# Optimization experiments

Measured on AMD Instinct MI355X. Metric: run time of the kernel, lower is better.

The kernel has to match this reference:

```python
import jax, jax.numpy as jnp
import numpy as np

N = 250_000          # total nodes
D = 256              # emb_size
B = 8_192            # number of graphs in batch


def setup_inputs() -> dict:
    key = jax.random.key(0)
    k1, k2, k3 = jax.random.split(key, 3)
    node_rep = jax.random.normal(k1, (N, D), dtype=jnp.float32)
    batch = jnp.sort(jax.random.randint(k2, (N,), 0, B, dtype=jnp.int32))
    # labels in [-1, 4); -1 marks 'condition' (reactant-context) nodes
    primary_label = jax.random.randint(k3, (N,), 0, 5, dtype=jnp.int32) - 1
    return {"node_rep": node_rep, "batch": batch,
            "primary_label": primary_label, "num_graphs": B}


def reference(node_rep, batch, primary_label, num_graphs):
    n = node_rep.shape[0]
    mask = primary_label == -1                              # [N] condition nodes
    maskf = mask.astype(node_rep.dtype)
    # segment mean of condition nodes per graph
    cond_sum = jax.ops.segment_sum(node_rep * maskf[:, None], batch,
                                   num_segments=num_graphs)         # [B, D]
    cond_cnt = jax.ops.segment_sum(maskf, batch, num_segments=num_graphs)  # [B]
    cond_mean = cond_sum / jnp.maximum(cond_cnt, 1.0)[:, None]
    # gate: pooled vector used only if the LAST node of the graph has label -1
    node_cnt = jax.ops.segment_sum(jnp.ones((n,), jnp.int32), batch,
                                   num_segments=num_graphs)          # [B]
    last_idx = jax.ops.segment_max(jnp.arange(n, dtype=jnp.int32), batch,
                                   num_segments=num_graphs)          # sorted batch
    last_idx = jnp.clip(last_idx, 0, n - 1)                          # guard empties
    gate = (primary_label[last_idx] == -1) & (node_cnt > 0)          # [B]
    cond_pool = jnp.where(gate[:, None], cond_mean, 0.0)             # [B, D]
    # broadcast pooled vector back to every node and concat -> [N, 2D]
    return jnp.concatenate([node_rep, cond_pool[batch]], axis=1)
```

## Files before the change

### kernel.cpp

```cpp
#include <hip/hip_runtime.h>


__global__ __launch_bounds__(256) void pool_kernel(
    const float* __restrict__ node_rep,
    const int*   __restrict__ batch,
    const int*   __restrict__ label,
    const int*   __restrict__ num_graphs,
    float*       __restrict__ pool,
    int n)
{
    const int g    = (blockIdx.x * blockDim.x + threadIdx.x) >> 6;
    const int lane = threadIdx.x & 63;
    const int B    = num_graphs[0];
    if (g >= B) return;

    int lo = 0, hi = n;
    while (lo < hi) { int mid = (lo + hi) >> 1; if (batch[mid] < g) lo = mid + 1; else hi = mid; }
    const int start = lo;
    hi = n;
    while (lo < hi) { int mid = (lo + hi) >> 1; if (batch[mid] < g + 1) lo = mid + 1; else hi = mid; }
    const int end = lo;

    const int col = lane << 2;
    float ax = 0.f, ay = 0.f, az = 0.f, aw = 0.f;
    int cnt = 0;
    for (int i = start; i < end; ++i) {
        if (label[i] == -1) {
            const float4 v = *reinterpret_cast<const float4*>(
                node_rep + (size_t)i * 256 + col);
            ax += v.x; ay += v.y; az += v.z; aw += v.w;
            ++cnt;
        }
    }
    const bool gate = (end > start) && (label[end - 1] == -1);
    const float inv = gate ? 1.0f / (float)(cnt > 0 ? cnt : 1) : 0.0f;
    float4 o;
    o.x = ax * inv; o.y = ay * inv; o.z = az * inv; o.w = aw * inv;
    *reinterpret_cast<float4*>(pool + (size_t)g * 256 + col) = o;
}

__global__ __launch_bounds__(256) void concat_kernel(
    const uint4* __restrict__ node4,
    const int*   __restrict__ batch,
    const uint4* __restrict__ pool4,
    uint4*       __restrict__ out4,
    int n)
{
    const int idx = blockIdx.x * blockDim.x + threadIdx.x;
    const int row = idx >> 7;
    const int c   = idx & 127;
    if (row >= n) return;
    uint4 v;
    if (c < 64) {
        v = node4[(size_t)row * 64 + c];
    } else {
        const int b = batch[row];
        v = pool4[(size_t)b * 64 + (c - 64)];
    }
    out4[(size_t)row * 128 + c] = v;
}

extern "C" void kernel_launch(void* const* d_in, const int* in_sizes, int n_in,
                              void* d_out, int out_size, void* d_ws, size_t ws_size,
                              hipStream_t stream) {
    const float* node_rep = (const float*)d_in[0];
    const int*   batch    = (const int*)d_in[1];
    const int*   label    = (const int*)d_in[2];
    const int*   num_g    = (const int*)d_in[3];
    const int    n        = in_sizes[1];
    const int    B_max    = 8192;

    float* pool = (float*)d_ws;

    {
        const int blocks = (B_max * 64 + 255) / 256;
        hipLaunchKernelGGL(pool_kernel, dim3(blocks), dim3(256), 0, stream,
                           node_rep, batch, label, num_g, pool, n);
    }
    {
        const long long threads = (long long)n * 128;
        const int blocks = (int)((threads + 255) / 256);
        hipLaunchKernelGGL(concat_kernel, dim3(blocks), dim3(256), 0, stream,
                           (const uint4*)node_rep, batch, (const uint4*)pool,
                           (uint4*)d_out, n);
    }
}
```

Baseline: 694.3 us.

## Fuse pooling and concat into one per-graph wavefront kernel

Merges the pooling and concatenation kernels into one kernel where each wavefront handles one graph. It reads every node row once, writes the left half of the output and accumulates the masked sum in the same pass, then writes the pooled vector to the right half of every node in the graph. Labels are loaded 64 at a time and turned into a ballot mask, and loads and stores use nontemporal hints. This drops the intermediate pool buffer, the second launch and the repeated read of node_rep. The cost is that each graph (about 30 rows) is walked serially by a single wavefront, which limits parallelism and memory-level concurrency.

Measured after the change: 683.7 us. No clear change (-1.5%).

```diff
diff --git a/kernel.cpp b/kernel.cpp
--- a/kernel.cpp
+++ b/kernel.cpp
@@ -1,63 +1,64 @@
 #include <hip/hip_runtime.h>
 
 
-__global__ __launch_bounds__(256) void pool_kernel(
-    const float* __restrict__ node_rep,
+typedef unsigned long long u64;
+typedef unsigned int u32x4 __attribute__((ext_vector_type(4)));
+typedef float        f32x4 __attribute__((ext_vector_type(4)));
+
+__global__ __launch_bounds__(256, 4) void fused_kernel(
+    const u32x4* __restrict__ node4,
     const int*   __restrict__ batch,
     const int*   __restrict__ label,
     const int*   __restrict__ num_graphs,
-    float*       __restrict__ pool,
+    u32x4*       __restrict__ out4,
     int n)
 {
-    const int g    = (blockIdx.x * blockDim.x + threadIdx.x) >> 6;
+    int g = (blockIdx.x * blockDim.x + threadIdx.x) >> 6;
+    g = __builtin_amdgcn_readfirstlane(g);
     const int lane = threadIdx.x & 63;
-    const int B    = num_graphs[0];
+    const int B = num_graphs[0];
     if (g >= B) return;
 
     int lo = 0, hi = n;
-    while (lo < hi) { int mid = (lo + hi) >> 1; if (batch[mid] < g) lo = mid + 1; else hi = mid; }
+    while (lo < hi) { int mid = (lo + hi) >> 1; if (batch[mid] < g)     lo = mid + 1; else hi = mid; }
     const int start = lo;
     hi = n;
     while (lo < hi) { int mid = (lo + hi) >> 1; if (batch[mid] < g + 1) lo = mid + 1; else hi = mid; }
     const int end = lo;
+    if (end <= start) return;
 
-    const int col = lane << 2;
+    const bool gate = (label[end - 1] == -1);
+
     float ax = 0.f, ay = 0.f, az = 0.f, aw = 0.f;
     int cnt = 0;
-    for (int i = start; i < end; ++i) {
-        if (label[i] == -1) {
-            const float4 v = *reinterpret_cast<const float4*>(
-                node_rep + (size_t)i * 256 + col);
-            ax += v.x; ay += v.y; az += v.z; aw += v.w;
-            ++cnt;
+
+    for (int base = start; base < end; base += 64) {
+        const int li  = base + lane;
+        const int lab = (li < end) ? label[li] : 0;
+        const u64 m   = __ballot(lab == -1);
+        cnt += __popcll(m);
+
+        const int nwin = min(64, end - base);
+        for (int j = 0; j < nwin; ++j) {
+            const size_t i = (size_t)(base + j);
+            const u32x4 v = __builtin_nontemporal_load(node4 + i * 64 + lane);
+            __builtin_nontemporal_store(v, out4 + i * 128 + lane);
+            const float s = (float)((unsigned)(m >> j) & 1u);
+            const f32x4 f = __builtin_bit_cast(f32x4, v);
+            ax = fmaf(s, f.x, ax);
+            ay = fmaf(s, f.y, ay);
+            az = fmaf(s, f.z, az);
+            aw = fmaf(s, f.w, aw);
         }
     }
-    const bool gate = (end > start) && (label[end - 1] == -1);
+
     const float inv = gate ? 1.0f / (float)(cnt > 0 ? cnt : 1) : 0.0f;
-    float4 o;
-    o.x = ax * inv; o.y = ay * inv; o.z = az * inv; o.w = aw * inv;
-    *reinterpret_cast<float4*>(pool + (size_t)g * 256 + col) = o;
-}
-
-__global__ __launch_bounds__(256) void concat_kernel(
-    const uint4* __restrict__ node4,
-    const int*   __restrict__ batch,
-    const uint4* __restrict__ pool4,
-    uint4*       __restrict__ out4,
-    int n)
-{
-    const int idx = blockIdx.x * blockDim.x + threadIdx.x;
-    const int row = idx >> 7;
-    const int c   = idx & 127;
-    if (row >= n) return;
-    uint4 v;
-    if (c < 64) {
-        v = node4[(size_t)row * 64 + c];
-    } else {
-        const int b = batch[row];
-        v = pool4[(size_t)b * 64 + (c - 64)];
+    f32x4 of;
+    of.x = ax * inv; of.y = ay * inv; of.z = az * inv; of.w = aw * inv;
+    const u32x4 o = __builtin_bit_cast(u32x4, of);
+    for (int i = start; i < end; ++i) {
+        __builtin_nontemporal_store(o, out4 + (size_t)i * 128 + 64 + lane);
     }
-    out4[(size_t)row * 128 + c] = v;
 }
 
 extern "C" void kernel_launch(void* const* d_in, const int* in_sizes, int n_in,
@@ -70,18 +71,8 @@
     const int    n        = in_sizes[1];
     const int    B_max    = 8192;
 
-    float* pool = (float*)d_ws;
-
-    {
-        const int blocks = (B_max * 64 + 255) / 256;
-        hipLaunchKernelGGL(pool_kernel, dim3(blocks), dim3(256), 0, stream,
-                           node_rep, batch, label, num_g, pool, n);
-    }
-    {
-        const long long threads = (long long)n * 128;
-        const int blocks = (int)((threads + 255) / 256);
-        hipLaunchKernelGGL(concat_kernel, dim3(blocks), dim3(256), 0, stream,
-                           (const uint4*)node_rep, batch, (const uint4*)pool,
-                           (uint4*)d_out, n);
-    }
+    const int blocks = (B_max * 64 + 255) / 256;
+    hipLaunchKernelGGL(fused_kernel, dim3(blocks), dim3(256), 0, stream,
+                       (const u32x4*)node_rep, batch, label, num_g,
+                       (u32x4*)d_out, n);
 }
```
